# Optimization experiments

Measured on AMD Instinct MI355X. Metric: run time of the kernel, lower is better.

## Reference

```python
import jax, jax.numpy as jnp
from jax import lax
import numpy as np

EPS = 1e-5
ALPHA = 0.2  # LeakyReLU slope


def setup_inputs() -> dict:
    key = jax.random.key(0)
    ks = jax.random.split(key, 8)
    B, N, F_IN, HID, OUT, H = 32, 512, 256, 512, 512, 4
    D = OUT // H
    return {
        "x": jax.random.normal(ks[0], (B, N, F_IN), dtype=jnp.float32),
        "adj": jax.random.uniform(ks[1], (N, N), dtype=jnp.float32),
        "gc_w": jax.random.normal(ks[2], (F_IN, HID), dtype=jnp.float32) * 0.04,
        "gc_b": jax.random.normal(ks[3], (HID,), dtype=jnp.float32) * 0.04,
        "bn1_g": jnp.ones((HID,), jnp.float32),
        "bn1_b": jnp.zeros((HID,), jnp.float32),
        "bn1_m": jnp.zeros((HID,), jnp.float32),
        "bn1_v": jnp.ones((HID,), jnp.float32),
        "gat_w": jax.random.normal(ks[4], (H, D, HID), dtype=jnp.float32) * 0.04,
        "conv_w": jax.random.normal(ks[5], (OUT, OUT, 3), dtype=jnp.float32) * 0.02,
        "conv_b": jax.random.normal(ks[6], (OUT,), dtype=jnp.float32) * 0.02,
        "bn2_g": jnp.ones((OUT,), jnp.float32),
        "bn2_b": jnp.zeros((OUT,), jnp.float32),
        "bn2_m": jnp.zeros((OUT,), jnp.float32),
        "bn2_v": jnp.ones((OUT,), jnp.float32),
    }


def reference(x, adj, gc_w, gc_b, bn1_g, bn1_b, bn1_m, bn1_v, gat_w,
              conv_w, conv_b, bn2_g, bn2_b, bn2_m, bn2_v):
    # --- GraphConvolution: adj @ (x @ W) + b ---
    support = jnp.einsum('bnc,cd->bnd', x, gc_w)
    g = jnp.einsum('nm,bmd->bnd', adj, support) + gc_b  # [B,N,HID]
    # --- BatchNorm1d over channel dim (eval mode) + ReLU ---
    g = (g - bn1_m) * (bn1_g / jnp.sqrt(bn1_v + EPS)) + bn1_b
    g = jax.nn.relu(g)
    # --- Multi-head GAT (repeat/mul/sum == attention-weighted matmul) ---
    hh = jnp.einsum('bnf,hdf->bhnd', g, gat_w)           # per-head projections
    e = jnp.einsum('bhnd,bhmd->bhnm', hh, hh)            # logits [B,H,N,N]
    e = jnp.where(e > 0, e, ALPHA * e)                   # LeakyReLU
    att = jax.nn.softmax(e, axis=-1)
    o = jnp.einsum('bhnm,bhmd->bhnd', att, hh)
    B, H, N, D = o.shape
    o = o.transpose(0, 2, 1, 3).reshape(B, N, H * D)     # concat heads [B,N,OUT]
    # --- TCN block: conv1d(k=3,pad=1) over node axis + BN(eval) + ReLU ---
    xc = o.transpose(0, 2, 1)                            # [B,C,N]
    y = lax.conv_general_dilated(xc, conv_w, (1,), ((1, 1),),
                                 dimension_numbers=('NCH', 'OIH', 'NCH'))
    y = y + conv_b[None, :, None]
    y = (y - bn2_m[None, :, None]) * (bn2_g / jnp.sqrt(bn2_v + EPS))[None, :, None] + bn2_b[None, :, None]
    y = jax.nn.relu(y)
    return y.transpose(0, 2, 1)                          # [B,N,OUT]
```

## Files before the change

kernel.cpp:

```cpp
#include <hip/hip_runtime.h>
#include <math.h>

#define BATCH 32
#define NNODE 512
#define FIN   256
#define HIDC  512
#define OUTC  512
#define NHEAD 4
#define HDIM  128
#define EPSV  1e-5f
#define ALPHA_LR 0.2f

typedef _Float16 half8 __attribute__((ext_vector_type(8)));
typedef _Float16 half4v __attribute__((ext_vector_type(4)));
typedef float floatx4 __attribute__((ext_vector_type(4)));

#define GLOBAL_TO_LDS16(g, l)                                                  \
  __builtin_amdgcn_global_load_lds(                                            \
      (const __attribute__((address_space(1))) void*)(g),                      \
      (__attribute__((address_space(3))) void*)(l), 16, 0, 0)

__device__ __forceinline__ void split_gemm_acc(
    const _Float16* __restrict__ Ah, const _Float16* __restrict__ Al, int lda,
    const _Float16* __restrict__ Bh, const _Float16* __restrict__ Bl, int ldb,
    int K, int rowBase, int colBase,
    _Float16* sAh, _Float16* sAl, _Float16* sBh, _Float16* sBl,
    floatx4 acc[4][4], int tid) {
  const int lane = tid & 63, wave = tid >> 6;
  const int wr = (wave >> 1) * 64, wc = (wave & 1) * 64;
  const int fr = lane & 15, q = lane >> 4;
  const int r = tid >> 2;
  const int cks = (((tid & 3) ^ ((r >> 1) & 3))) * 8;
  const int qx = (q ^ ((fr >> 1) & 3)) * 8;
  for (int k0 = 0; k0 < K; k0 += 64) {
#pragma unroll
    for (int s = 0; s < 2; ++s) {
      const int kc = k0 + s * 32;
      const int o = s * 4096;
      GLOBAL_TO_LDS16(&Ah[(size_t)(rowBase + r) * lda + kc + cks], &sAh[o + tid * 8]);
      GLOBAL_TO_LDS16(&Ah[(size_t)(rowBase + r + 64) * lda + kc + cks], &sAh[o + 2048 + tid * 8]);
      GLOBAL_TO_LDS16(&Al[(size_t)(rowBase + r) * lda + kc + cks], &sAl[o + tid * 8]);
      GLOBAL_TO_LDS16(&Al[(size_t)(rowBase + r + 64) * lda + kc + cks], &sAl[o + 2048 + tid * 8]);
      GLOBAL_TO_LDS16(&Bh[(size_t)(colBase + r) * ldb + kc + cks], &sBh[o + tid * 8]);
      GLOBAL_TO_LDS16(&Bh[(size_t)(colBase + r + 64) * ldb + kc + cks], &sBh[o + 2048 + tid * 8]);
      GLOBAL_TO_LDS16(&Bl[(size_t)(colBase + r) * ldb + kc + cks], &sBl[o + tid * 8]);
      GLOBAL_TO_LDS16(&Bl[(size_t)(colBase + r + 64) * ldb + kc + cks], &sBl[o + 2048 + tid * 8]);
    }
    __syncthreads();
#pragma unroll
    for (int s = 0; s < 2; ++s) {
      const int o = s * 4096;
      half8 ah[4], al4[4], bh[4], bl4[4];
#pragma unroll
      for (int i = 0; i < 4; ++i) {
        ah[i]  = *(const half8*)&sAh[o + (wr + i * 16 + fr) * 32 + qx];
        al4[i] = *(const half8*)&sAl[o + (wr + i * 16 + fr) * 32 + qx];
      }
#pragma unroll
      for (int j = 0; j < 4; ++j) {
        bh[j]  = *(const half8*)&sBh[o + (wc + j * 16 + fr) * 32 + qx];
        bl4[j] = *(const half8*)&sBl[o + (wc + j * 16 + fr) * 32 + qx];
      }
#pragma unroll
      for (int i = 0; i < 4; ++i)
#pragma unroll
        for (int j = 0; j < 4; ++j) {
          acc[i][j] = __builtin_amdgcn_mfma_f32_16x16x32_f16(al4[i], bh[j], acc[i][j], 0, 0, 0);
          acc[i][j] = __builtin_amdgcn_mfma_f32_16x16x32_f16(ah[i], bl4[j], acc[i][j], 0, 0, 0);
          acc[i][j] = __builtin_amdgcn_mfma_f32_16x16x32_f16(ah[i], bh[j], acc[i][j], 0, 0, 0);
        }
    }
    __syncthreads();
  }
}

__global__ __launch_bounds__(256) void k_prep(
    const float* __restrict__ adj, const float* __restrict__ gcw,
    const float* __restrict__ gatw, const float* __restrict__ cw,
    _Float16* __restrict__ ADJh, _Float16* __restrict__ ADJl,
    _Float16* __restrict__ GWh, _Float16* __restrict__ GWl,
    _Float16* __restrict__ GAh, _Float16* __restrict__ GAl,
    _Float16* __restrict__ WT, _Float16* __restrict__ OP) {
  const int i = blockIdx.x * 256 + threadIdx.x;
  if (i < 262144) {
    float v = adj[i];
    _Float16 h = (_Float16)v;
    ADJh[i] = h; ADJl[i] = (_Float16)(v - (float)h);
  } else if (i < 393216) {
    int j = i - 262144;
    int n = j >> 8, k = j & 255;
    float v = gcw[(size_t)k * HIDC + n];
    _Float16 h = (_Float16)v;
    GWh[j] = h; GWl[j] = (_Float16)(v - (float)h);
  } else if (i < 655360) {
    int j = i - 393216;
    float v = gatw[j];
    _Float16 h = (_Float16)v;
    GAh[j] = h; GAl[j] = (_Float16)(v - (float)h);
  } else if (i < 1441792) {
    int j = i - 655360;
    int n = j / 1536, kk = j - n * 1536;
    int tap = kk >> 9, ci = kk & 511;
    WT[j] = (_Float16)cw[(size_t)n * 1536 + ci * 3 + tap];
  } else if (i < 1474560) {
    int j = i - 1441792;
    int b = j >> 10, rs = (j >> 9) & 1, c = j & 511;
    OP[((size_t)b * 514 + rs * 513) * OUTC + c] = (_Float16)0.f;
  }
}

__global__ __launch_bounds__(256) void k_xsplit_t(const float* __restrict__ X,
                                                  _Float16* __restrict__ XTh,
                                                  _Float16* __restrict__ XTl) {
  __shared__ float sT[64][65];
  const int bt = blockIdx.x;
  const int ft = bt & 3;
  const int mt = (bt >> 2) & 7;
  const int b  = bt >> 5;
  const int tid = threadIdx.x;
  const int rr = tid >> 4, cc4 = (tid & 15) * 4;
#pragma unroll
  for (int it = 0; it < 4; ++it) {
    int m = rr + it * 16;
    float4 v = *(const float4*)&X[((size_t)(b * 512 + mt * 64 + m)) * 256 + ft * 64 + cc4];
    sT[m][cc4] = v.x; sT[m][cc4 + 1] = v.y; sT[m][cc4 + 2] = v.z; sT[m][cc4 + 3] = v.w;
  }
  __syncthreads();
#pragma unroll
  for (int it = 0; it < 4; ++it) {
    int f = rr + it * 16;
    half4v h, l;
#pragma unroll
    for (int e = 0; e < 4; ++e) {
      float v = sT[cc4 + e][f];
      _Float16 hh = (_Float16)v;
      h[e] = hh; l[e] = (_Float16)(v - (float)hh);
    }
    size_t base = ((size_t)b * 256 + ft * 64 + f) * 512 + mt * 64 + cc4;
    *(half4v*)&XTh[base] = h;
    *(half4v*)&XTl[base] = l;
  }
}

__global__ __launch_bounds__(256) void k_ax(
    const _Float16* __restrict__ ADJh, const _Float16* __restrict__ ADJl,
    const _Float16* __restrict__ XTh, const _Float16* __restrict__ XTl,
    _Float16* __restrict__ AXh, _Float16* __restrict__ AXl) {
  __shared__ _Float16 sAh[8192], sAl[8192], sBh[4096], sBl[4096];
  const int tid = threadIdx.x;
  const int lane = tid & 63, wave = tid >> 6;
  const int fr = lane & 15, q = lane >> 4;
  const int r = tid >> 2;
  const int cks = (((tid & 3) ^ ((r >> 1) & 3))) * 8;
  const int qx = (q ^ ((fr >> 1) & 3)) * 8;
  const int id = blockIdx.y * 4 + blockIdx.x;
  const int jj = id >> 3;
  const int rowBase = ((id & 7) * 16 + (jj >> 2)) * 128;
  const int colBase = (jj & 3) * 64;
  const int b = rowBase >> 9;
  const int nrow = rowBase & 511;
  const _Float16* Bh = XTh + (size_t)b * FIN * NNODE;
  const _Float16* Bl = XTl + (size_t)b * FIN * NNODE;
  floatx4 acc[2][4] = {};
  for (int k0 = 0; k0 < NNODE; k0 += 64) {
#pragma unroll
    for (int s = 0; s < 2; ++s) {
      const int kc = k0 + s * 32;
      const int oA = s * 4096, oB = s * 2048;
      GLOBAL_TO_LDS16(&ADJh[(size_t)(nrow + r) * NNODE + kc + cks], &sAh[oA + tid * 8]);
      GLOBAL_TO_LDS16(&ADJh[(size_t)(nrow + r + 64) * NNODE + kc + cks], &sAh[oA + 2048 + tid * 8]);
      GLOBAL_TO_LDS16(&ADJl[(size_t)(nrow + r) * NNODE + kc + cks], &sAl[oA + tid * 8]);
      GLOBAL_TO_LDS16(&ADJl[(size_t)(nrow + r + 64) * NNODE + kc + cks], &sAl[oA + 2048 + tid * 8]);
      GLOBAL_TO_LDS16(&Bh[(size_t)(colBase + r) * NNODE + kc + cks], &sBh[oB + tid * 8]);
      GLOBAL_TO_LDS16(&Bl[(size_t)(colBase + r) * NNODE + kc + cks], &sBl[oB + tid * 8]);
    }
    __syncthreads();
#pragma unroll
    for (int s = 0; s < 2; ++s) {
      const int oA = s * 4096, oB = s * 2048;
      half8 ah[2], al4[2], bh[4], bl4[4];
#pragma unroll
      for (int i = 0; i < 2; ++i) {
        ah[i]  = *(const half8*)&sAh[oA + (wave * 32 + i * 16 + fr) * 32 + qx];
        al4[i] = *(const half8*)&sAl[oA + (wave * 32 + i * 16 + fr) * 32 + qx];
      }
#pragma unroll
      for (int j = 0; j < 4; ++j) {
        bh[j]  = *(const half8*)&sBh[oB + (j * 16 + fr) * 32 + qx];
        bl4[j] = *(const half8*)&sBl[oB + (j * 16 + fr) * 32 + qx];
      }
#pragma unroll
      for (int i = 0; i < 2; ++i)
#pragma unroll
        for (int j = 0; j < 4; ++j) {
          acc[i][j] = __builtin_amdgcn_mfma_f32_16x16x32_f16(al4[i], bh[j], acc[i][j], 0, 0, 0);
          acc[i][j] = __builtin_amdgcn_mfma_f32_16x16x32_f16(ah[i], bl4[j], acc[i][j], 0, 0, 0);
          acc[i][j] = __builtin_amdgcn_mfma_f32_16x16x32_f16(ah[i], bh[j], acc[i][j], 0, 0, 0);
        }
    }
    __syncthreads();
  }
#pragma unroll
  for (int i = 0; i < 2; ++i) {
    const int r0 = rowBase + wave * 32 + i * 16 + q * 4;
#pragma unroll
    for (int rg = 0; rg < 4; ++rg) {
      size_t base = (size_t)(r0 + rg) * FIN + colBase + fr;
#pragma unroll
      for (int j = 0; j < 4; ++j) {
        float v = acc[i][j][rg];
        _Float16 h = (_Float16)v;
        AXh[base + j * 16] = h;
        AXl[base + j * 16] = (_Float16)(v - (float)h);
      }
    }
  }
}

__global__ __launch_bounds__(256) void k_gcn2(
    const _Float16* __restrict__ AXh, const _Float16* __restrict__ AXl,
    const _Float16* __restrict__ GWh, const _Float16* __restrict__ GWl,
    const float* __restrict__ gcb, const float* __restrict__ g1,
    const float* __restrict__ b1, const float* __restrict__ m1,
    const float* __restrict__ v1,
    _Float16* __restrict__ Gh, _Float16* __restrict__ Gl) {
  __shared__ _Float16 sm[4][8192];
  const int tid = threadIdx.x;
  const int id = blockIdx.y * 4 + blockIdx.x;
  const int jj = id >> 3;
  const int rowBase = ((id & 7) * 16 + (jj >> 2)) * 128;
  const int colBase = (jj & 3) * 128;
  floatx4 acc[4][4] = {};
  split_gemm_acc(AXh, AXl, FIN, GWh, GWl, FIN, FIN, rowBase, colBase,
                 sm[0], sm[1], sm[2], sm[3], acc, tid);
  const int lane = tid & 63, wave = tid >> 6;
  const int wr = (wave >> 1) * 64, wc = (wave & 1) * 64;
  const int fr = lane & 15, q = lane >> 4;
  float sc[4], of[4];
#pragma unroll
  for (int j = 0; j < 4; ++j) {
    int c = colBase + wc + j * 16 + fr;
    float s = g1[c] * rsqrtf(v1[c] + EPSV);
    sc[j] = s;
    of[j] = (gcb[c] - m1[c]) * s + b1[c];
  }
#pragma unroll
  for (int i = 0; i < 4; ++i) {
    const int r0 = rowBase + wr + i * 16 + q * 4;
#pragma unroll
    for (int rg = 0; rg < 4; ++rg) {
      size_t base = (size_t)(r0 + rg) * HIDC + colBase + wc + fr;
#pragma unroll
      for (int j = 0; j < 4; ++j) {
        float v = fmaxf(fmaf(acc[i][j][rg], sc[j], of[j]), 0.0f);
        _Float16 h = (_Float16)v;
        Gh[base + j * 16] = h;
        Gl[base + j * 16] = (_Float16)(v - (float)h);
      }
    }
  }
}

__global__ __launch_bounds__(256) void k_hh(
    const _Float16* __restrict__ Gh, const _Float16* __restrict__ Gl,
    const _Float16* __restrict__ GAh, const _Float16* __restrict__ GAl,
    _Float16* __restrict__ HHh, _Float16* __restrict__ HHl,
    _Float16* __restrict__ HHT) {
  __shared__ _Float16 sm[4][8192];
  const int tid = threadIdx.x;
  const int id = blockIdx.y * 4 + blockIdx.x;
  const int jj = id >> 3;
  const int rowBase = ((id & 7) * 16 + (jj >> 2)) * 128;
  const int colBase = (jj & 3) * 128;
  floatx4 acc[4][4] = {};
  split_gemm_acc(Gh, Gl, HIDC, GAh, GAl, HIDC, HIDC, rowBase, colBase,
                 sm[0], sm[1], sm[2], sm[3], acc, tid);
  const int lane = tid & 63, wave = tid >> 6;
  const int wr = (wave >> 1) * 64, wc = (wave & 1) * 64;
  const int fr = lane & 15, q = lane >> 4;
#pragma unroll
  for (int i = 0; i < 4; ++i) {
    const int r0 = rowBase + wr + i * 16 + q * 4;
    const int node = r0 & 511;
    const int bbv = r0 >> 9;
#pragma unroll
    for (int j = 0; j < 4; ++j) {
      const int c = colBase + wc + j * 16 + fr;
      half4v v4;
#pragma unroll
      for (int rg = 0; rg < 4; ++rg) {
        float v = acc[i][j][rg];
        _Float16 h = (_Float16)v;
        size_t base = (size_t)(r0 + rg) * OUTC + c;
        HHh[base] = h;
        HHl[base] = (_Float16)(v - (float)h);
        v4[rg] = h;
      }
      if (HHT)
        *(half4v*)&HHT[((size_t)(bbv * 4 + (c >> 7)) * 128 + (c & 127)) * 512 + node] = v4;
    }
  }
}

__global__ __launch_bounds__(256) void k_vt(const _Float16* __restrict__ HHh,
                                            _Float16* __restrict__ HHT) {
  __shared__ _Float16 sT[128 * 132];
  const int bt = blockIdx.x;
  const int nt = bt & 3, g = bt >> 2;
  const int bb = g >> 2, h = g & 3;
  const int tid = threadIdx.x;
  const int rr = tid >> 4, cc = (tid & 15) * 8;
#pragma unroll
  for (int it = 0; it < 8; ++it) {
    int node = rr + it * 16;
    half8 v = *(const half8*)&HHh[((size_t)bb * 512 + nt * 128 + node) * 512 + h * 128 + cc];
#pragma unroll
    for (int e = 0; e < 8; ++e) sT[(cc + e) * 132 + node] = v[e];
  }
  __syncthreads();
#pragma unroll
  for (int it = 0; it < 8; ++it) {
    int d = rr + it * 16;
    half8 v;
#pragma unroll
    for (int e = 0; e < 8; ++e) v[e] = sT[d * 132 + cc + e];
    *(half8*)&HHT[((size_t)g * 128 + d) * 512 + nt * 128 + cc] = v;
  }
}

__global__ __launch_bounds__(256, 2) void k_attn(
    const _Float16* __restrict__ HHh, const _Float16* __restrict__ HHl,
    const _Float16* __restrict__ HHT, _Float16* __restrict__ OP) {
  __shared__ _Float16 sK[8][2048];
  __shared__ _Float16 sP[128 * 68];
  _Float16* sV = &sK[0][0];
  const int tid = threadIdx.x;
  const int lane = tid & 63, wave = tid >> 6;
  const int fr = lane & 15, q = lane >> 4;
  const int id = blockIdx.x;
  const int slot = id >> 3;
  const int g = (id & 7) + 8 * (slot >> 2);
  const int qBase = (slot & 3) * 128;
  const int bb = g >> 2, h = g & 3;
  const int w32 = wave * 32;
  const _Float16* Qh = HHh + (size_t)bb * NNODE * OUTC + h * HDIM;
  const _Float16* Ql = HHl + (size_t)bb * NNODE * OUTC + h * HDIM;
  const _Float16* VT = HHT + (size_t)g * HDIM * NNODE;
  const int rk = tid >> 2;
  const int cks = (((tid & 3) ^ ((rk >> 1) & 3))) * 8;
  const int qx = (q ^ ((fr >> 1) & 3)) * 8;

  half8 qh[2][4], ql[2][4];
#pragma unroll
  for (int m = 0; m < 2; ++m)
#pragma unroll
    for (int k0 = 0; k0 < 4; ++k0) {
      const size_t off = (size_t)(qBase + w32 + m * 16 + fr) * OUTC + k0 * 32 + q * 8;
      qh[m][k0] = *(const half8*)&Qh[off];
      ql[m][k0] = *(const half8*)&Ql[off];
    }

  floatx4 oacc[2][8] = {};
  float m_i[2][4], l_i[2][4];
#pragma unroll
  for (int m = 0; m < 2; ++m)
#pragma unroll
    for (int rg = 0; rg < 4; ++rg) { m_i[m][rg] = -1e30f; l_i[m][rg] = 0.f; }

  for (int kt = 0; kt < 8; ++kt) {
    const int ktb = kt * 64;
#pragma unroll
    for (int t = 0; t < 4; ++t) {
      GLOBAL_TO_LDS16(&Qh[(size_t)(ktb + rk) * OUTC + t * 32 + cks], &sK[t][tid * 8]);
      GLOBAL_TO_LDS16(&Ql[(size_t)(ktb + rk) * OUTC + t * 32 + cks], &sK[4 + t][tid * 8]);
    }
    __syncthreads();
    floatx4 sacc[2][4] = {};
#pragma unroll
    for (int k0 = 0; k0 < 4; ++k0)
#pragma unroll
      for (int j = 0; j < 4; ++j) {
        half8 bh = *(const half8*)&sK[k0][(j * 16 + fr) * 32 + qx];
        half8 bl = *(const half8*)&sK[4 + k0][(j * 16 + fr) * 32 + qx];
#pragma unroll
        for (int m = 0; m < 2; ++m) {
          sacc[m][j] = __builtin_amdgcn_mfma_f32_16x16x32_f16(ql[m][k0], bh, sacc[m][j], 0, 0, 0);
          sacc[m][j] = __builtin_amdgcn_mfma_f32_16x16x32_f16(qh[m][k0], bl, sacc[m][j], 0, 0, 0);
          sacc[m][j] = __builtin_amdgcn_mfma_f32_16x16x32_f16(qh[m][k0], bh, sacc[m][j], 0, 0, 0);
        }
      }
    __syncthreads();
#pragma unroll
    for (int m = 0; m < 2; ++m) {
#pragma unroll
      for (int j = 0; j < 4; ++j)
#pragma unroll
        for (int rg = 0; rg < 4; ++rg) {
          float v = sacc[m][j][rg];
          sacc[m][j][rg] = v > 0.f ? v : ALPHA_LR * v;
        }
#pragma unroll
      for (int rg = 0; rg < 4; ++rg) {
        float mx = sacc[m][0][rg];
#pragma unroll
        for (int j = 1; j < 4; ++j) mx = fmaxf(mx, sacc[m][j][rg]);
        mx = fmaxf(mx, __shfl_xor(mx, 1));
        mx = fmaxf(mx, __shfl_xor(mx, 2));
        mx = fmaxf(mx, __shfl_xor(mx, 4));
        mx = fmaxf(mx, __shfl_xor(mx, 8));
        float mnew = fmaxf(m_i[m][rg], mx);
        float alpha = __expf(m_i[m][rg] - mnew);
        m_i[m][rg] = mnew;
        float sum = 0.f;
#pragma unroll
        for (int j = 0; j < 4; ++j) {
          float p = __expf(sacc[m][j][rg] - mnew);
          sacc[m][j][rg] = p;
          sum += p;
        }
        sum += __shfl_xor(sum, 1);
        sum += __shfl_xor(sum, 2);
        sum += __shfl_xor(sum, 4);
        sum += __shfl_xor(sum, 8);
        l_i[m][rg] = l_i[m][rg] * alpha + sum;
#pragma unroll
        for (int j = 0; j < 8; ++j) oacc[m][j][rg] *= alpha;
      }
    }
#pragma unroll
    for (int l = 0; l < 4; ++l)
      GLOBAL_TO_LDS16(&VT[(size_t)((l >> 1) * 64 + rk) * NNODE + ktb + (l & 1) * 32 + cks],
                      &sV[(l & 1) * 4096 + (l >> 1) * 2048 + tid * 8]);
#pragma unroll
    for (int m = 0; m < 2; ++m)
#pragma unroll
      for (int j = 0; j < 4; ++j)
#pragma unroll
        for (int rg = 0; rg < 4; ++rg)
          sP[(w32 + m * 16 + q * 4 + rg) * 68 + j * 16 + fr] = (_Float16)sacc[m][j][rg];
    __syncthreads();
#pragma unroll
    for (int ks = 0; ks < 2; ++ks) {
      half8 pa0 = *(const half8*)&sP[(w32 + fr) * 68 + ks * 32 + q * 8];
      half8 pa1 = *(const half8*)&sP[(w32 + 16 + fr) * 68 + ks * 32 + q * 8];
#pragma unroll
      for (int j = 0; j < 8; ++j) {
        half8 bv = *(const half8*)&sV[ks * 4096 + (j * 16 + fr) * 32 + qx];
        oacc[0][j] = __builtin_amdgcn_mfma_f32_16x16x32_f16(pa0, bv, oacc[0][j], 0, 0, 0);
        oacc[1][j] = __builtin_amdgcn_mfma_f32_16x16x32_f16(pa1, bv, oacc[1][j], 0, 0, 0);
      }
    }
    __syncthreads();
  }
#pragma unroll
  for (int m = 0; m < 2; ++m)
#pragma unroll
    for (int rg = 0; rg < 4; ++rg) {
      const float inv = 1.0f / l_i[m][rg];
      const int node = qBase + w32 + m * 16 + q * 4 + rg;
      size_t base = ((size_t)bb * 514 + 1 + node) * OUTC + h * HDIM + fr;
#pragma unroll
      for (int j = 0; j < 8; ++j)
        OP[base + j * 16] = (_Float16)(oacc[m][j][rg] * inv);
    }
}

__global__ __launch_bounds__(256) void k_conv_mfma(
    const _Float16* __restrict__ OP, const _Float16* __restrict__ WT,
    const float* __restrict__ cb, const float* __restrict__ g2,
    const float* __restrict__ b2, const float* __restrict__ m2,
    const float* __restrict__ v2, float* __restrict__ Y) {
  __shared__ _Float16 At[8192];
  __shared__ _Float16 Bt[8192];
  const int tid = threadIdx.x;
  const int lane = tid & 63, wave = tid >> 6;
  const int wr = (wave >> 1) * 64, wc = (wave & 1) * 64;
  const int id = blockIdx.y * 4 + blockIdx.x;
  const int jj = id >> 3;
  const int rowBase = ((id & 7) * 16 + (jj >> 2)) * 128;
  const int colBase = (jj & 3) * 128;
  const int b = rowBase >> 9;
  const int n0 = rowBase & 511;
  const int r = tid >> 2;
  const int cks = (((tid & 3) ^ ((r >> 1) & 3))) * 8;
  const int fr = lane & 15, q = lane >> 4;
  const int qx = (q ^ ((fr >> 1) & 3)) * 8;
  floatx4 acc[4][4] = {};
  for (int k0 = 0; k0 < 3 * OUTC; k0 += 64) {
#pragma unroll
    for (int s = 0; s < 2; ++s) {
      const int kc = k0 + s * 32;
      const int o = s * 4096;
      const int tap = kc >> 9;
      const int cib = kc & 511;
      const size_t abase = ((size_t)b * 514 + n0 + tap) * OUTC + cib + cks;
      GLOBAL_TO_LDS16(&OP[abase + (size_t)r * OUTC],        &At[o + tid * 8]);
      GLOBAL_TO_LDS16(&OP[abase + (size_t)(r + 64) * OUTC], &At[o + 2048 + tid * 8]);
      GLOBAL_TO_LDS16(&WT[(size_t)(colBase + r) * 1536 + kc + cks],      &Bt[o + tid * 8]);
      GLOBAL_TO_LDS16(&WT[(size_t)(colBase + r + 64) * 1536 + kc + cks], &Bt[o + 2048 + tid * 8]);
    }
    __syncthreads();
#pragma unroll
    for (int s = 0; s < 2; ++s) {
      const int o = s * 4096;
      half8 af[4], bf[4];
#pragma unroll
      for (int i = 0; i < 4; ++i)
        af[i] = *(const half8*)&At[o + (wr + i * 16 + fr) * 32 + qx];
#pragma unroll
      for (int j = 0; j < 4; ++j)
        bf[j] = *(const half8*)&Bt[o + (wc + j * 16 + fr) * 32 + qx];
#pragma unroll
      for (int i = 0; i < 4; ++i)
#pragma unroll
        for (int j = 0; j < 4; ++j)
          acc[i][j] = __builtin_amdgcn_mfma_f32_16x16x32_f16(af[i], bf[j], acc[i][j], 0, 0, 0);
    }
    __syncthreads();
  }
  float sc[4], of[4];
#pragma unroll
  for (int j = 0; j < 4; ++j) {
    int c = colBase + wc + j * 16 + fr;
    float s = g2[c] * rsqrtf(v2[c] + EPSV);
    sc[j] = s;
    of[j] = (cb[c] - m2[c]) * s + b2[c];
  }
#pragma unroll
  for (int i = 0; i < 4; ++i) {
    const int R0r = rowBase + wr + i * 16 + q * 4;
#pragma unroll
    for (int rg = 0; rg < 4; ++rg) {
      float* dst = &Y[(size_t)(R0r + rg) * OUTC + colBase + wc + fr];
#pragma unroll
      for (int j = 0; j < 4; ++j)
        dst[j * 16] = fmaxf(fmaf(acc[i][j][rg], sc[j], of[j]), 0.0f);
    }
  }
}

extern "C" void kernel_launch(void* const* d_in, const int* in_sizes, int n_in,
                              void* d_out, int out_size, void* d_ws, size_t ws_size,
                              hipStream_t stream) {
  const float* x     = (const float*)d_in[0];
  const float* adj   = (const float*)d_in[1];
  const float* gc_w  = (const float*)d_in[2];
  const float* gc_b  = (const float*)d_in[3];
  const float* bn1_g = (const float*)d_in[4];
  const float* bn1_b = (const float*)d_in[5];
  const float* bn1_m = (const float*)d_in[6];
  const float* bn1_v = (const float*)d_in[7];
  const float* gat_w = (const float*)d_in[8];
  const float* conv_w= (const float*)d_in[9];
  const float* conv_b= (const float*)d_in[10];
  const float* bn2_g = (const float*)d_in[11];
  const float* bn2_b = (const float*)d_in[12];
  const float* bn2_m = (const float*)d_in[13];
  const float* bn2_v = (const float*)d_in[14];
  float* out = (float*)d_out;

  char* ws = (char*)d_ws;
  _Float16* AXh = (_Float16*)(ws + 0);
  _Float16* AXl = (_Float16*)(ws + 16777216);
  _Float16* HHh = (_Float16*)(ws + 0);
  _Float16* HHl = (_Float16*)(ws + 16777216);
  _Float16* XTh = (_Float16*)(ws + 33554432);
  _Float16* XTl = (_Float16*)(ws + 41943040);
  _Float16* Gh  = (_Float16*)(ws + 33554432);
  _Float16* Gl  = (_Float16*)(ws + 50331648);
  _Float16* OP  = (_Float16*)(ws + 67108864);
  _Float16* WT  = (_Float16*)(ws + 83951616);
  _Float16* ADJh= (_Float16*)(ws + 85524480);
  _Float16* ADJl= (_Float16*)(ws + 86048768);
  _Float16* GWh = (_Float16*)(ws + 86573056);
  _Float16* GWl = (_Float16*)(ws + 86835200);
  _Float16* GAh = (_Float16*)(ws + 87097344);
  _Float16* GAl = (_Float16*)(ws + 87621632);

  const bool fused = ws_size >= (size_t)(88145920 + 16777216);
  _Float16* HHT = fused ? (_Float16*)(ws + 88145920)
                        : (_Float16*)(ws + 33554432);

  k_prep<<<5760, 256, 0, stream>>>(adj, gc_w, gat_w, conv_w,
                                   ADJh, ADJl, GWh, GWl, GAh, GAl, WT, OP);
  k_xsplit_t<<<1024, 256, 0, stream>>>(x, XTh, XTl);
  k_ax<<<dim3(4, 128), 256, 0, stream>>>(ADJh, ADJl, XTh, XTl, AXh, AXl);
  k_gcn2<<<dim3(4, 128), 256, 0, stream>>>(AXh, AXl, GWh, GWl, gc_b,
                                           bn1_g, bn1_b, bn1_m, bn1_v, Gh, Gl);
  if (fused) {
    k_hh<<<dim3(4, 128), 256, 0, stream>>>(Gh, Gl, GAh, GAl, HHh, HHl, HHT);
  } else {
    k_hh<<<dim3(4, 128), 256, 0, stream>>>(Gh, Gl, GAh, GAl, HHh, HHl,
                                           (_Float16*)nullptr);
    k_vt<<<512, 256, 0, stream>>>(HHh, HHT);
  }
  k_attn<<<512, 256, 0, stream>>>(HHh, HHl, HHT, OP);
  k_conv_mfma<<<dim3(4, 128), 256, 0, stream>>>(OP, WT, conv_b,
                                                bn2_g, bn2_b, bn2_m, bn2_v, out);
}
```

Measured before the change: 260.1 us.

## Merge x split into prep kernel and skip lazy softmax rescales

Folds the x transpose/split kernel into k_prep as extra blocks, which removes one kernel launch. In the flash-attention loop, each tile's running max is only updated when some row's new max exceeds the old one by more than 8. Otherwise the per-row alpha exp and the rescale of the output accumulators are skipped. Staying within that threshold keeps exponentials bounded near e^8 in fp32, but fp16 P values could overflow past the half range of 65504. That is a numerical accuracy risk.

```diff
diff --git a/kernel.cpp b/kernel.cpp
--- a/kernel.cpp
+++ b/kernel.cpp
@@ -77,10 +77,43 @@
 __global__ __launch_bounds__(256) void k_prep(
     const float* __restrict__ adj, const float* __restrict__ gcw,
     const float* __restrict__ gatw, const float* __restrict__ cw,
+    const float* __restrict__ X,
     _Float16* __restrict__ ADJh, _Float16* __restrict__ ADJl,
     _Float16* __restrict__ GWh, _Float16* __restrict__ GWl,
     _Float16* __restrict__ GAh, _Float16* __restrict__ GAl,
-    _Float16* __restrict__ WT, _Float16* __restrict__ OP) {
+    _Float16* __restrict__ WT, _Float16* __restrict__ OP,
+    _Float16* __restrict__ XTh, _Float16* __restrict__ XTl) {
+  if (blockIdx.x >= 5760) {
+    __shared__ float sT[64][65];
+    const int bt = blockIdx.x - 5760;
+    const int ft = bt & 3;
+    const int mt = (bt >> 2) & 7;
+    const int b  = bt >> 5;
+    const int tid = threadIdx.x;
+    const int rr = tid >> 4, cc4 = (tid & 15) * 4;
+#pragma unroll
+    for (int it = 0; it < 4; ++it) {
+      int m = rr + it * 16;
+      float4 v = *(const float4*)&X[((size_t)(b * 512 + mt * 64 + m)) * 256 + ft * 64 + cc4];
+      sT[m][cc4] = v.x; sT[m][cc4 + 1] = v.y; sT[m][cc4 + 2] = v.z; sT[m][cc4 + 3] = v.w;
+    }
+    __syncthreads();
+#pragma unroll
+    for (int it = 0; it < 4; ++it) {
+      int f = rr + it * 16;
+      half4v h, l;
+#pragma unroll
+      for (int e = 0; e < 4; ++e) {
+        float v = sT[cc4 + e][f];
+        _Float16 hh = (_Float16)v;
+        h[e] = hh; l[e] = (_Float16)(v - (float)hh);
+      }
+      size_t base = ((size_t)b * 256 + ft * 64 + f) * 512 + mt * 64 + cc4;
+      *(half4v*)&XTh[base] = h;
+      *(half4v*)&XTl[base] = l;
+    }
+    return;
+  }
   const int i = blockIdx.x * 256 + threadIdx.x;
   if (i < 262144) {
     float v = adj[i];
@@ -109,39 +142,6 @@
   }
 }
 
-__global__ __launch_bounds__(256) void k_xsplit_t(const float* __restrict__ X,
-                                                  _Float16* __restrict__ XTh,
-                                                  _Float16* __restrict__ XTl) {
-  __shared__ float sT[64][65];
-  const int bt = blockIdx.x;
-  const int ft = bt & 3;
-  const int mt = (bt >> 2) & 7;
-  const int b  = bt >> 5;
-  const int tid = threadIdx.x;
-  const int rr = tid >> 4, cc4 = (tid & 15) * 4;
-#pragma unroll
-  for (int it = 0; it < 4; ++it) {
-    int m = rr + it * 16;
-    float4 v = *(const float4*)&X[((size_t)(b * 512 + mt * 64 + m)) * 256 + ft * 64 + cc4];
-    sT[m][cc4] = v.x; sT[m][cc4 + 1] = v.y; sT[m][cc4 + 2] = v.z; sT[m][cc4 + 3] = v.w;
-  }
-  __syncthreads();
-#pragma unroll
-  for (int it = 0; it < 4; ++it) {
-    int f = rr + it * 16;
-    half4v h, l;
-#pragma unroll
-    for (int e = 0; e < 4; ++e) {
-      float v = sT[cc4 + e][f];
-      _Float16 hh = (_Float16)v;
-      h[e] = hh; l[e] = (_Float16)(v - (float)hh);
-    }
-    size_t base = ((size_t)b * 256 + ft * 64 + f) * 512 + mt * 64 + cc4;
-    *(half4v*)&XTh[base] = h;
-    *(half4v*)&XTl[base] = l;
-  }
-}
-
 __global__ __launch_bounds__(256) void k_ax(
     const _Float16* __restrict__ ADJh, const _Float16* __restrict__ ADJl,
     const _Float16* __restrict__ XTh, const _Float16* __restrict__ XTl,
@@ -399,6 +399,8 @@
           float v = sacc[m][j][rg];
           sacc[m][j][rg] = v > 0.f ? v : ALPHA_LR * v;
         }
+      float mxv[4];
+      int need = 0;
 #pragma unroll
       for (int rg = 0; rg < 4; ++rg) {
         float mx = sacc[m][0][rg];
@@ -408,23 +410,46 @@
         mx = fmaxf(mx, __shfl_xor(mx, 2));
         mx = fmaxf(mx, __shfl_xor(mx, 4));
         mx = fmaxf(mx, __shfl_xor(mx, 8));
-        float mnew = fmaxf(m_i[m][rg], mx);
-        float alpha = __expf(m_i[m][rg] - mnew);
-        m_i[m][rg] = mnew;
-        float sum = 0.f;
-#pragma unroll
-        for (int j = 0; j < 4; ++j) {
-          float p = __expf(sacc[m][j][rg] - mnew);
-          sacc[m][j][rg] = p;
-          sum += p;
+        mxv[rg] = mx;
+        need |= (mx > m_i[m][rg] + 8.0f) ? 1 : 0;
+      }
+      if (__ballot(need) != 0ULL) {
+#pragma unroll
+        for (int rg = 0; rg < 4; ++rg) {
+          float mnew = fmaxf(m_i[m][rg], mxv[rg]);
+          float alpha = __expf(m_i[m][rg] - mnew);
+          m_i[m][rg] = mnew;
+          float sum = 0.f;
+#pragma unroll
+          for (int j = 0; j < 4; ++j) {
+            float p = __expf(sacc[m][j][rg] - mnew);
+            sacc[m][j][rg] = p;
+            sum += p;
+          }
+          sum += __shfl_xor(sum, 1);
+          sum += __shfl_xor(sum, 2);
+          sum += __shfl_xor(sum, 4);
+          sum += __shfl_xor(sum, 8);
+          l_i[m][rg] = l_i[m][rg] * alpha + sum;
+#pragma unroll
+          for (int j = 0; j < 8; ++j) oacc[m][j][rg] *= alpha;
         }
-        sum += __shfl_xor(sum, 1);
-        sum += __shfl_xor(sum, 2);
-        sum += __shfl_xor(sum, 4);
-        sum += __shfl_xor(sum, 8);
-        l_i[m][rg] = l_i[m][rg] * alpha + sum;
-#pragma unroll
-        for (int j = 0; j < 8; ++j) oacc[m][j][rg] *= alpha;
+      } else {
+#pragma unroll
+        for (int rg = 0; rg < 4; ++rg) {
+          float sum = 0.f;
+#pragma unroll
+          for (int j = 0; j < 4; ++j) {
+            float p = __expf(sacc[m][j][rg] - m_i[m][rg]);
+            sacc[m][j][rg] = p;
+            sum += p;
+          }
+          sum += __shfl_xor(sum, 1);
+          sum += __shfl_xor(sum, 2);
+          sum += __shfl_xor(sum, 4);
+          sum += __shfl_xor(sum, 8);
+          l_i[m][rg] += sum;
+        }
       }
     }
 #pragma unroll
@@ -581,9 +606,9 @@
   _Float16* HHT = fused ? (_Float16*)(ws + 88145920)
                         : (_Float16*)(ws + 33554432);
 
-  k_prep<<<5760, 256, 0, stream>>>(adj, gc_w, gat_w, conv_w,
-                                   ADJh, ADJl, GWh, GWl, GAh, GAl, WT, OP);
-  k_xsplit_t<<<1024, 256, 0, stream>>>(x, XTh, XTl);
+  k_prep<<<6784, 256, 0, stream>>>(adj, gc_w, gat_w, conv_w, x,
+                                   ADJh, ADJl, GWh, GWl, GAh, GAl, WT, OP,
+                                   XTh, XTl);
   k_ax<<<dim3(4, 128), 256, 0, stream>>>(ADJh, ADJl, XTh, XTl, AXh, AXl);
   k_gcn2<<<dim3(4, 128), 256, 0, stream>>>(AXh, AXl, GWh, GWl, gc_b,
                                            bn1_g, bn1_b, bn1_m, bn1_v, Gh, Gl);
```

Result: slower. 271.4 us (+4.3%).
